# Optimization experiments

Hardware: AMD Instinct MI355X
Metric: run time of the kernel (lower is better)

## Reference

```python
import jax, jax.numpy as jnp
import numpy as np

D_MODEL = 256
B, S = 4, 4096


def setup_inputs() -> dict:
    key = jax.random.key(0)
    ks = jax.random.split(key, 6)
    k = jax.random.normal(ks[0], (B, S, D_MODEL), dtype=jnp.float32)
    q = jax.random.normal(ks[1], (B, S, D_MODEL), dtype=jnp.float32)
    v = jax.random.normal(ks[2], (B, S, D_MODEL), dtype=jnp.float32)
    # causal mask: (S, S), 1 where attending is allowed, 0 elsewhere
    mask = jnp.tril(jnp.ones((S, S), dtype=jnp.int32))
    # nn.Linear(d, d, bias=False) weights, applied as x @ W.T
    scale = 1.0 / np.sqrt(D_MODEL)
    Wk = jax.random.uniform(ks[3], (D_MODEL, D_MODEL), jnp.float32, -scale, scale)
    Wq = jax.random.uniform(ks[4], (D_MODEL, D_MODEL), jnp.float32, -scale, scale)
    Wv = jax.random.uniform(ks[5], (D_MODEL, D_MODEL), jnp.float32, -scale, scale)
    return {"k": k, "q": q, "v": v, "Wk": Wk, "Wq": Wq, "Wv": Wv, "mask": mask}


def reference(k, q, v, Wk, Wq, Wv, mask):
    # projections: nn.Linear applies x @ W.T
    key = jnp.einsum('bsd,ed->bse', k, Wk)
    query = jnp.einsum('bsd,ed->bse', q, Wq)
    value = jnp.einsum('bsd,ed->bse', v, Wv)
    # scores (b, s_q, s_k), scaled by sqrt(d_model)
    logits = jnp.einsum('bqd,bkd->bqk', query, key) / jnp.sqrt(jnp.float32(query.shape[-1]))
    logits = jnp.where(mask[None, :, :] == 0, -jnp.inf, logits)
    probs = jax.nn.softmax(logits, axis=-1)
    # dropout p=0.0 (eval) -> identity
    return jnp.einsum('bqk,bkd->bqd', probs, value)
```

## Files before the change

### kernel.cpp

```cpp
#include <hip/hip_runtime.h>


typedef __bf16 bf16_t;
typedef bf16_t bf16x8 __attribute__((ext_vector_type(8)));
typedef bf16_t bf16x4 __attribute__((ext_vector_type(4)));
typedef float  f32x4  __attribute__((ext_vector_type(4)));
typedef float  f32x16 __attribute__((ext_vector_type(16)));
typedef unsigned int u32;
typedef u32 u32x4 __attribute__((ext_vector_type(4)));

#define MFMA16(a, b, c) __builtin_amdgcn_mfma_f32_16x16x32_bf16((a), (b), (c), 0, 0, 0)
#define MFMA32(a, b, c) __builtin_amdgcn_mfma_f32_32x32x16_bf16((a), (b), (c), 0, 0, 0)

#define GLOAD_LDS16(gsrc, ldst) \
    __builtin_amdgcn_global_load_lds( \
        (const __attribute__((address_space(1))) void*)(gsrc), \
        (__attribute__((address_space(3))) void*)(ldst), 16, 0, 0)

#define NB      4
#define SEQ     4096
#define DM      256
#define NROWS   (NB * SEQ)
#define NELEM   ((size_t)NROWS * DM)
#define QSCALE  0.09016844005556021f
#define DEFER_THR 8.0f
#define SPLITG  4

__device__ __forceinline__ int swz(int row, int bytecol) {
    return bytecol ^ ((row & 7) << 4);
}

__device__ __forceinline__ u32 packbf(float a, float b) {
    union { bf16_t h; unsigned short s; } ca, cb;
    ca.h = (bf16_t)a; cb.h = (bf16_t)b;
    return (u32)ca.s | ((u32)cb.s << 16);
}

__device__ __forceinline__ bf16x8 u4_to_b8(u32x4 u) {
    union { u32x4 u; bf16x8 b; } cv; cv.u = u; return cv.b;
}

__global__ __launch_bounds__(256) void proj_kernel(
    const float* __restrict__ qin, const float* __restrict__ kin,
    const float* __restrict__ vin,
    const float* __restrict__ Wq, const float* __restrict__ Wk,
    const float* __restrict__ Wv,
    bf16_t* __restrict__ Qb, bf16_t* __restrict__ Kb, bf16_t* __restrict__ Vt)
{
    __shared__ char a_lds[128 * 64 * 2];
    __shared__ char w_lds[128 * 64 * 2];

    const int z = blockIdx.z;
    const float* in = (z == 0) ? qin : (z == 1) ? kin : vin;
    const float* W  = (z == 0) ? Wq  : (z == 1) ? Wk  : Wv;

    const int m0 = blockIdx.x * 128;
    const int n0 = blockIdx.y * 128;
    const int tid = threadIdx.x;
    const int l  = tid & 63;
    const int w  = tid >> 6;
    const int wr = w >> 1, wc = w & 1;
    const int lg = l >> 4, cl = l & 15;

    f32x4 acc[4][4] = {};

    for (int k0 = 0; k0 < DM; k0 += 64) {
#pragma unroll
        for (int i = 0; i < 8; ++i) {
            int chunk = tid + i * 256;
            int row = chunk >> 4;
            int kk  = (chunk & 15) * 4;
            float4 av = *(const float4*)(in + (size_t)(m0 + row) * DM + k0 + kk);
            bf16x4 ap;
            ap[0] = (bf16_t)av.x; ap[1] = (bf16_t)av.y;
            ap[2] = (bf16_t)av.z; ap[3] = (bf16_t)av.w;
            *(bf16x4*)(a_lds + row * 128 + swz(row, kk * 2)) = ap;

            float4 wv4 = *(const float4*)(W + (size_t)(n0 + row) * DM + k0 + kk);
            bf16x4 wp;
            wp[0] = (bf16_t)wv4.x; wp[1] = (bf16_t)wv4.y;
            wp[2] = (bf16_t)wv4.z; wp[3] = (bf16_t)wv4.w;
            *(bf16x4*)(w_lds + row * 128 + swz(row, kk * 2)) = wp;
        }
        __syncthreads();

#pragma unroll
        for (int ks = 0; ks < 2; ++ks) {
            bf16x8 af[4], bfr[4];
#pragma unroll
            for (int mi = 0; mi < 4; ++mi) {
                int row = wr * 64 + mi * 16 + cl;
                int kb2 = (ks * 32 + lg * 8) * 2;
                af[mi] = *(bf16x8*)(a_lds + row * 128 + swz(row, kb2));
            }
#pragma unroll
            for (int ni = 0; ni < 4; ++ni) {
                int row = wc * 64 + ni * 16 + cl;
                int kb2 = (ks * 32 + lg * 8) * 2;
                bfr[ni] = *(bf16x8*)(w_lds + row * 128 + swz(row, kb2));
            }
#pragma unroll
            for (int mi = 0; mi < 4; ++mi)
#pragma unroll
                for (int ni = 0; ni < 4; ++ni)
                    acc[mi][ni] = MFMA16(af[mi], bfr[ni], acc[mi][ni]);
        }
        __syncthreads();
    }

#pragma unroll
    for (int mi = 0; mi < 4; ++mi) {
#pragma unroll
        for (int ni = 0; ni < 4; ++ni) {
            int mbase = m0 + wr * 64 + mi * 16 + lg * 4;
            int ncol  = n0 + wc * 64 + ni * 16 + cl;
            if (z == 0) {
#pragma unroll
                for (int i = 0; i < 4; ++i)
                    Qb[(size_t)(mbase + i) * DM + ncol] = (bf16_t)(acc[mi][ni][i] * QSCALE);
            } else if (z == 1) {
#pragma unroll
                for (int i = 0; i < 4; ++i)
                    Kb[(size_t)(mbase + i) * DM + ncol] = (bf16_t)acc[mi][ni][i];
            } else {
                int bb = mbase >> 12;
                int s0 = mbase & 4095;
                bf16x4 pk;
                pk[0] = (bf16_t)acc[mi][ni][0]; pk[1] = (bf16_t)acc[mi][ni][1];
                pk[2] = (bf16_t)acc[mi][ni][2]; pk[3] = (bf16_t)acc[mi][ni][3];
                *(bf16x4*)(Vt + ((size_t)bb << 20) + (size_t)ncol * SEQ + s0) = pk;
            }
        }
    }
}

__global__ __launch_bounds__(128, 2) void attn_kernel(
    const bf16_t* __restrict__ Qb, const bf16_t* __restrict__ Kb,
    const bf16_t* __restrict__ Vt,
    float* __restrict__ O0, bf16_t* __restrict__ O1, float* __restrict__ ML)
{
    __shared__ __attribute__((aligned(16))) char smem[2 * 16384];

    const int g = blockIdx.x;
    const int xcd = g & 7;
    const int b = xcd >> 1;
    const int idx = ((g >> 3) << 1) | (xcd & 1);
    const int p = idx & 63;
    const int sblk = idx >> 6;

    const int tid = threadIdx.x;
    const int dhalf = tid >> 6;
    const int l = tid & 63;
    const int q5 = l & 31;
    const int hi = l >> 5;
    const int dbase = dhalf * 128;

    char* cur = smem;
    char* nxt = smem + 16384;

    const int segc[2] = { p, 127 - p };

    auto stageK = [&](int t, char* dst) {
        const size_t rbase = (size_t)(b * SEQ) + (size_t)t * 32;
#pragma unroll
        for (int i = 0; i < 8; ++i) {
            int chunk = i * 128 + tid;
            int row = chunk >> 5;
            int bc  = (chunk & 31) << 4;
            int scol = bc ^ ((row & 15) << 4);
            GLOAD_LDS16(Kb + (rbase + row) * DM + (scol >> 1), dst + chunk * 16);
        }
    };

    for (int sg = 0; sg < 2; ++sg) {
        const int c = segc[sg];
        const int qbase = c * 32;
        const int nt = c + 1;
        const int T0 = (nt * sblk) / SPLITG;
        const int T1 = (nt * (sblk + 1)) / SPLITG;
        const int qg = qbase + q5;

        __syncthreads();

        const bf16_t* qrow = Qb + (size_t)(b * SEQ + qg) * DM + hi * 8;
        bf16x8 qf[16];
#pragma unroll
        for (int ks = 0; ks < 16; ++ks)
            qf[ks] = *(const bf16x8*)(qrow + ks * 16);

        f32x16 o[4] = {};
        float m_ = -1e30f, ssum = 0.0f;

        if (T0 < T1) stageK(T0, cur);

        for (int t = T0; t < T1; ++t) {
            const int kv0 = t * 32;
            __syncthreads();

            if (t + 1 < T1) stageK(t + 1, nxt);

            const bf16_t* vbase = Vt + ((size_t)b << 20) + kv0 + hi * 8;
            bf16x8 vreg[8];
#pragma unroll
            for (int db = 0; db < 4; ++db) {
                const bf16_t* vr = vbase + (size_t)(dbase + db * 32 + q5) * SEQ;
                vreg[2 * db]     = *(const bf16x8*)(vr);
                vreg[2 * db + 1] = *(const bf16x8*)(vr + 16);
            }

            f32x16 sA = {}, sB = {};
#pragma unroll
            for (int ks = 0; ks < 16; ++ks) {
                bf16x8 kf = *(bf16x8*)(cur + q5 * 512 +
                                       ((ks * 32 + hi * 16) ^ ((q5 & 15) << 4)));
                if (ks & 1) sB = MFMA32(kf, qf[ks], sB);
                else        sA = MFMA32(kf, qf[ks], sA);
            }
            f32x16 sv = sA + sB;

            if (t == c) {
#pragma unroll
                for (int r = 0; r < 16; ++r) {
                    int kv = kv0 + (r & 3) + 8 * (r >> 2) + 4 * hi;
                    if (kv > qg) sv[r] = -1e30f;
                }
            }

            float rm = sv[0];
#pragma unroll
            for (int r = 1; r < 16; ++r) rm = fmaxf(rm, sv[r]);
            rm = fmaxf(rm, __shfl_xor(rm, 32));
            float mn = (rm > m_ + DEFER_THR) ? rm : m_;
            float al = exp2f(m_ - mn);
            m_ = mn;
            float rs = 0.0f;
#pragma unroll
            for (int r = 0; r < 16; ++r) { sv[r] = exp2f(sv[r] - mn); rs += sv[r]; }
            rs += __shfl_xor(rs, 32);
            ssum = ssum * al + rs;
            if (al != 1.0f) {
#pragma unroll
                for (int db = 0; db < 4; ++db) o[db] *= al;
            }

            u32 cpk[8], spk[8];
#pragma unroll
            for (int j = 0; j < 8; ++j) cpk[j] = packbf(sv[2 * j], sv[2 * j + 1]);
#pragma unroll
            for (int j = 0; j < 8; ++j) spk[j] = (u32)__shfl_xor((int)cpk[j], 32);
            u32x4 f0, f1;
            f0[0] = hi ? spk[2] : cpk[0];
            f0[1] = hi ? spk[3] : cpk[1];
            f0[2] = hi ? cpk[2] : spk[0];
            f0[3] = hi ? cpk[3] : spk[1];
            f1[0] = hi ? spk[6] : cpk[4];
            f1[1] = hi ? spk[7] : cpk[5];
            f1[2] = hi ? cpk[6] : spk[4];
            f1[3] = hi ? cpk[7] : spk[5];
            bf16x8 pb0 = u4_to_b8(f0);
            bf16x8 pb1 = u4_to_b8(f1);

#pragma unroll
            for (int db = 0; db < 4; ++db) {
                o[db] = MFMA32(vreg[2 * db],     pb0, o[db]);
                o[db] = MFMA32(vreg[2 * db + 1], pb1, o[db]);
            }

            char* tmp = cur; cur = nxt; nxt = tmp;
        }

        const size_t row = (size_t)(b * SEQ + qg);
        if (sblk == 0) {
#pragma unroll
            for (int db = 0; db < 4; ++db)
#pragma unroll
                for (int rr = 0; rr < 4; ++rr) {
                    int d = dbase + db * 32 + rr * 8 + hi * 4;
                    f32x4 v4 = { o[db][rr * 4 + 0], o[db][rr * 4 + 1],
                                 o[db][rr * 4 + 2], o[db][rr * 4 + 3] };
                    *(f32x4*)(O0 + row * DM + d) = v4;
                }
        } else {
            bf16_t* O1s = O1 + (size_t)(sblk - 1) * NELEM;
#pragma unroll
            for (int db = 0; db < 4; ++db)
#pragma unroll
                for (int rr = 0; rr < 4; ++rr) {
                    int d = dbase + db * 32 + rr * 8 + hi * 4;
                    bf16x4 v4;
                    v4[0] = (bf16_t)o[db][rr * 4 + 0];
                    v4[1] = (bf16_t)o[db][rr * 4 + 1];
                    v4[2] = (bf16_t)o[db][rr * 4 + 2];
                    v4[3] = (bf16_t)o[db][rr * 4 + 3];
                    *(bf16x4*)(O1s + row * DM + d) = v4;
                }
        }
        if (dhalf == 0 && hi == 0) {
            ML[(row * SPLITG + sblk) * 2 + 0] = m_;
            ML[(row * SPLITG + sblk) * 2 + 1] = ssum;
        }
    }
}

__global__ __launch_bounds__(256) void combine_kernel(
    const float* __restrict__ O0, const bf16_t* __restrict__ O1,
    const float* __restrict__ ML, float* __restrict__ out, int split)
{
    const int row = blockIdx.x * 4 + (threadIdx.x >> 6);
    const int l = threadIdx.x & 63;
    const float* mlr = ML + (size_t)row * split * 2;

    float M = -1e30f;
    for (int s = 0; s < split; ++s) M = fmaxf(M, mlr[s * 2]);
    float denom = 0.0f;
    for (int s = 0; s < split; ++s) denom += exp2f(mlr[s * 2] - M) * mlr[s * 2 + 1];
    const float inv = 1.0f / denom;

    const float w0 = exp2f(mlr[0] - M);
    f32x4 a = *(const f32x4*)(O0 + (size_t)row * DM + l * 4);
    f32x4 acc;
#pragma unroll
    for (int j = 0; j < 4; ++j) acc[j] = w0 * a[j];
    for (int s = 1; s < split; ++s) {
        float wss = exp2f(mlr[s * 2] - M);
        bf16x4 bv = *(const bf16x4*)(O1 + (size_t)(s - 1) * NELEM +
                                     (size_t)row * DM + l * 4);
#pragma unroll
        for (int j = 0; j < 4; ++j) acc[j] += wss * (float)bv[j];
    }
    f32x4 r;
#pragma unroll
    for (int j = 0; j < 4; ++j) r[j] = acc[j] * inv;
    *(f32x4*)(out + (size_t)row * DM + l * 4) = r;
}

extern "C" void kernel_launch(void* const* d_in, const int* in_sizes, int n_in,
                              void* d_out, int out_size, void* d_ws, size_t ws_size,
                              hipStream_t stream) {
    const float* k_in = (const float*)d_in[0];
    const float* q_in = (const float*)d_in[1];
    const float* v_in = (const float*)d_in[2];
    const float* Wk   = (const float*)d_in[3];
    const float* Wq   = (const float*)d_in[4];
    const float* Wv   = (const float*)d_in[5];

    bf16_t* Qb = (bf16_t*)d_ws;
    bf16_t* Kb = Qb + NELEM;
    bf16_t* Vt = Kb + NELEM;
    bf16_t* O1 = Vt + NELEM;
    float*  ML = (float*)(O1 + (size_t)(SPLITG - 1) * NELEM);
    float* outp = (float*)d_out;

    proj_kernel<<<dim3(NROWS / 128, DM / 128, 3), 256, 0, stream>>>(
        q_in, k_in, v_in, Wq, Wk, Wv, Qb, Kb, Vt);
    attn_kernel<<<4 * 64 * SPLITG, 128, 0, stream>>>(Qb, Kb, Vt, outp, O1, ML);
    combine_kernel<<<NROWS / 4, 256, 0, stream>>>(outp, O1, ML, outp, SPLITG);
}
```

Baseline: 139.6 us.

## Share K tiles across two query sub-blocks per 256-thread block, raise split

The attention block grows from 128 to 256 threads so each block covers 64 query rows (two 32-row sub-blocks) and shares each staged K tile in LDS between them, halving K staging per query row. The KV split becomes a runtime parameter, set to 8 when the workspace is large enough, which keeps the grid size up despite the bigger blocks. The cost is wasted iterations for the lower query sub-block on the last tile, a heavier combine pass with more partial outputs to read, and tighter register pressure under launch_bounds(256,4).

```diff
diff --git a/kernel.cpp b/kernel.cpp
--- a/kernel.cpp
+++ b/kernel.cpp
@@ -24,7 +24,6 @@
 #define NELEM   ((size_t)NROWS * DM)
 #define QSCALE  0.09016844005556021f
 #define DEFER_THR 8.0f
-#define SPLITG  4
 
 __device__ __forceinline__ int swz(int row, int bytecol) {
     return bytecol ^ ((row & 7) << 4);
@@ -134,10 +133,11 @@
     }
 }
 
-__global__ __launch_bounds__(128, 2) void attn_kernel(
+__global__ __launch_bounds__(256, 4) void attn_kernel(
     const bf16_t* __restrict__ Qb, const bf16_t* __restrict__ Kb,
     const bf16_t* __restrict__ Vt,
-    float* __restrict__ O0, bf16_t* __restrict__ O1, float* __restrict__ ML)
+    float* __restrict__ O0, bf16_t* __restrict__ O1, float* __restrict__ ML,
+    int split)
 {
     __shared__ __attribute__((aligned(16))) char smem[2 * 16384];
 
@@ -145,11 +145,13 @@
     const int xcd = g & 7;
     const int b = xcd >> 1;
     const int idx = ((g >> 3) << 1) | (xcd & 1);
-    const int p = idx & 63;
-    const int sblk = idx >> 6;
+    const int p = idx & 31;
+    const int sblk = idx >> 5;
 
     const int tid = threadIdx.x;
-    const int dhalf = tid >> 6;
+    const int w = tid >> 6;
+    const int qsub  = w >> 1;
+    const int dhalf = w & 1;
     const int l = tid & 63;
     const int q5 = l & 31;
     const int hi = l >> 5;
@@ -158,13 +160,13 @@
     char* cur = smem;
     char* nxt = smem + 16384;
 
-    const int segc[2] = { p, 127 - p };
+    const int segc[2] = { p, 31 - p + 32 };
 
     auto stageK = [&](int t, char* dst) {
         const size_t rbase = (size_t)(b * SEQ) + (size_t)t * 32;
 #pragma unroll
-        for (int i = 0; i < 8; ++i) {
-            int chunk = i * 128 + tid;
+        for (int i = 0; i < 4; ++i) {
+            int chunk = i * 256 + tid;
             int row = chunk >> 5;
             int bc  = (chunk & 31) << 4;
             int scol = bc ^ ((row & 15) << 4);
@@ -174,10 +176,11 @@
 
     for (int sg = 0; sg < 2; ++sg) {
         const int c = segc[sg];
-        const int qbase = c * 32;
-        const int nt = c + 1;
-        const int T0 = (nt * sblk) / SPLITG;
-        const int T1 = (nt * (sblk + 1)) / SPLITG;
+        const int nt = 2 * c + 2;
+        const int T0 = (nt * sblk) / split;
+        const int T1 = (nt * (sblk + 1)) / split;
+        const int ntw = 2 * c + 1 + qsub;
+        const int qbase = c * 64 + qsub * 32;
         const int qg = qbase + q5;
 
         __syncthreads();
@@ -199,71 +202,73 @@
 
             if (t + 1 < T1) stageK(t + 1, nxt);
 
-            const bf16_t* vbase = Vt + ((size_t)b << 20) + kv0 + hi * 8;
-            bf16x8 vreg[8];
-#pragma unroll
-            for (int db = 0; db < 4; ++db) {
-                const bf16_t* vr = vbase + (size_t)(dbase + db * 32 + q5) * SEQ;
-                vreg[2 * db]     = *(const bf16x8*)(vr);
-                vreg[2 * db + 1] = *(const bf16x8*)(vr + 16);
-            }
-
-            f32x16 sA = {}, sB = {};
-#pragma unroll
-            for (int ks = 0; ks < 16; ++ks) {
-                bf16x8 kf = *(bf16x8*)(cur + q5 * 512 +
-                                       ((ks * 32 + hi * 16) ^ ((q5 & 15) << 4)));
-                if (ks & 1) sB = MFMA32(kf, qf[ks], sB);
-                else        sA = MFMA32(kf, qf[ks], sA);
-            }
-            f32x16 sv = sA + sB;
-
-            if (t == c) {
-#pragma unroll
-                for (int r = 0; r < 16; ++r) {
-                    int kv = kv0 + (r & 3) + 8 * (r >> 2) + 4 * hi;
-                    if (kv > qg) sv[r] = -1e30f;
-                }
-            }
-
-            float rm = sv[0];
-#pragma unroll
-            for (int r = 1; r < 16; ++r) rm = fmaxf(rm, sv[r]);
-            rm = fmaxf(rm, __shfl_xor(rm, 32));
-            float mn = (rm > m_ + DEFER_THR) ? rm : m_;
-            float al = exp2f(m_ - mn);
-            m_ = mn;
-            float rs = 0.0f;
-#pragma unroll
-            for (int r = 0; r < 16; ++r) { sv[r] = exp2f(sv[r] - mn); rs += sv[r]; }
-            rs += __shfl_xor(rs, 32);
-            ssum = ssum * al + rs;
-            if (al != 1.0f) {
-#pragma unroll
-                for (int db = 0; db < 4; ++db) o[db] *= al;
-            }
-
-            u32 cpk[8], spk[8];
-#pragma unroll
-            for (int j = 0; j < 8; ++j) cpk[j] = packbf(sv[2 * j], sv[2 * j + 1]);
-#pragma unroll
-            for (int j = 0; j < 8; ++j) spk[j] = (u32)__shfl_xor((int)cpk[j], 32);
-            u32x4 f0, f1;
-            f0[0] = hi ? spk[2] : cpk[0];
-            f0[1] = hi ? spk[3] : cpk[1];
-            f0[2] = hi ? cpk[2] : spk[0];
-            f0[3] = hi ? cpk[3] : spk[1];
-            f1[0] = hi ? spk[6] : cpk[4];
-            f1[1] = hi ? spk[7] : cpk[5];
-            f1[2] = hi ? cpk[6] : spk[4];
-            f1[3] = hi ? cpk[7] : spk[5];
-            bf16x8 pb0 = u4_to_b8(f0);
-            bf16x8 pb1 = u4_to_b8(f1);
-
-#pragma unroll
-            for (int db = 0; db < 4; ++db) {
-                o[db] = MFMA32(vreg[2 * db],     pb0, o[db]);
-                o[db] = MFMA32(vreg[2 * db + 1], pb1, o[db]);
+            if (t < ntw) {
+                const bf16_t* vbase = Vt + ((size_t)b << 20) + kv0 + hi * 8;
+                bf16x8 vreg[8];
+#pragma unroll
+                for (int db = 0; db < 4; ++db) {
+                    const bf16_t* vr = vbase + (size_t)(dbase + db * 32 + q5) * SEQ;
+                    vreg[2 * db]     = *(const bf16x8*)(vr);
+                    vreg[2 * db + 1] = *(const bf16x8*)(vr + 16);
+                }
+
+                f32x16 sA = {}, sB = {};
+#pragma unroll
+                for (int ks = 0; ks < 16; ++ks) {
+                    bf16x8 kf = *(bf16x8*)(cur + q5 * 512 +
+                                           ((ks * 32 + hi * 16) ^ ((q5 & 15) << 4)));
+                    if (ks & 1) sB = MFMA32(kf, qf[ks], sB);
+                    else        sA = MFMA32(kf, qf[ks], sA);
+                }
+                f32x16 sv = sA + sB;
+
+                if (t == ntw - 1) {
+#pragma unroll
+                    for (int r = 0; r < 16; ++r) {
+                        int kv = kv0 + (r & 3) + 8 * (r >> 2) + 4 * hi;
+                        if (kv > qg) sv[r] = -1e30f;
+                    }
+                }
+
+                float rm = sv[0];
+#pragma unroll
+                for (int r = 1; r < 16; ++r) rm = fmaxf(rm, sv[r]);
+                rm = fmaxf(rm, __shfl_xor(rm, 32));
+                float mn = (rm > m_ + DEFER_THR) ? rm : m_;
+                float al = exp2f(m_ - mn);
+                m_ = mn;
+                float rs = 0.0f;
+#pragma unroll
+                for (int r = 0; r < 16; ++r) { sv[r] = exp2f(sv[r] - mn); rs += sv[r]; }
+                rs += __shfl_xor(rs, 32);
+                ssum = ssum * al + rs;
+                if (al != 1.0f) {
+#pragma unroll
+                    for (int db = 0; db < 4; ++db) o[db] *= al;
+                }
+
+                u32 cpk[8], spk[8];
+#pragma unroll
+                for (int j = 0; j < 8; ++j) cpk[j] = packbf(sv[2 * j], sv[2 * j + 1]);
+#pragma unroll
+                for (int j = 0; j < 8; ++j) spk[j] = (u32)__shfl_xor((int)cpk[j], 32);
+                u32x4 f0, f1;
+                f0[0] = hi ? spk[2] : cpk[0];
+                f0[1] = hi ? spk[3] : cpk[1];
+                f0[2] = hi ? cpk[2] : spk[0];
+                f0[3] = hi ? cpk[3] : spk[1];
+                f1[0] = hi ? spk[6] : cpk[4];
+                f1[1] = hi ? spk[7] : cpk[5];
+                f1[2] = hi ? cpk[6] : spk[4];
+                f1[3] = hi ? cpk[7] : spk[5];
+                bf16x8 pb0 = u4_to_b8(f0);
+                bf16x8 pb1 = u4_to_b8(f1);
+
+#pragma unroll
+                for (int db = 0; db < 4; ++db) {
+                    o[db] = MFMA32(vreg[2 * db],     pb0, o[db]);
+                    o[db] = MFMA32(vreg[2 * db + 1], pb1, o[db]);
+                }
             }
 
             char* tmp = cur; cur = nxt; nxt = tmp;
@@ -296,8 +301,8 @@
                 }
         }
         if (dhalf == 0 && hi == 0) {
-            ML[(row * SPLITG + sblk) * 2 + 0] = m_;
-            ML[(row * SPLITG + sblk) * 2 + 1] = ssum;
+            ML[(row * split + sblk) * 2 + 0] = m_;
+            ML[(row * split + sblk) * 2 + 1] = ssum;
         }
     }
 }
@@ -344,15 +349,18 @@
     const float* Wq   = (const float*)d_in[4];
     const float* Wv   = (const float*)d_in[5];
 
+    const size_t need8 = NELEM * 2 * 10 + (size_t)NROWS * 8 * 2 * sizeof(float);
+    const int split = (ws_size >= need8) ? 8 : 4;
+
     bf16_t* Qb = (bf16_t*)d_ws;
     bf16_t* Kb = Qb + NELEM;
     bf16_t* Vt = Kb + NELEM;
     bf16_t* O1 = Vt + NELEM;
-    float*  ML = (float*)(O1 + (size_t)(SPLITG - 1) * NELEM);
+    float*  ML = (float*)(O1 + (size_t)(split - 1) * NELEM);
     float* outp = (float*)d_out;
 
     proj_kernel<<<dim3(NROWS / 128, DM / 128, 3), 256, 0, stream>>>(
         q_in, k_in, v_in, Wq, Wk, Wv, Qb, Kb, Vt);
-    attn_kernel<<<4 * 64 * SPLITG, 128, 0, stream>>>(Qb, Kb, Vt, outp, O1, ML);
-    combine_kernel<<<NROWS / 4, 256, 0, stream>>>(outp, O1, ML, outp, SPLITG);
-}
+    attn_kernel<<<128 * split, 256, 0, stream>>>(Qb, Kb, Vt, outp, O1, ML, split);
+    combine_kernel<<<NROWS / 4, 256, 0, stream>>>(outp, O1, ML, outp, split);
+}
```

Result: slower. 397.9 us (+185.1%).
